# Kernel optimization log

Measured on AMD Instinct MI355X. Metric: run time of the kernel, lower is better.

Reference implementation:

```python
import jax, jax.numpy as jnp
import numpy as np

# __init__ hyperparameters (defaults)
TRACE_BINS = 24
SMOOTH_KERNEL = 5
PAUSE_ENERGY_STD = -0.5
PAUSE_DELTA_Q = 0.35
VOICED_STD = -0.1
BOUNDARY_Q = 0.75

B, T, MEL = 64, 8000, 80


def _sliding_mean(x, k):
    """avg_pool1d(stride=1, padding=k//2, count_include_pad=True) via cumsum. x: [B,T]."""
    pad = k // 2
    xp = jnp.pad(x, ((0, 0), (pad, pad)))
    c = jnp.pad(jnp.cumsum(xp, axis=1), ((0, 0), (1, 0)))
    return (c[:, k:] - c[:, :-k]) / k


def _run_mean(mask):
    """Mean length of runs of True in mask [B,T] = (#ones)/(#runs), 0 if no runs."""
    prev_off = jnp.pad(~mask[:, :-1], ((0, 0), (1, 0)), constant_values=True)
    starts = mask & prev_off
    n_runs = starts.sum(axis=1).astype(jnp.float32)
    ones = mask.sum(axis=1).astype(jnp.float32)
    return jnp.where(n_runs > 0, ones / jnp.maximum(n_runs, 1.0), 0.0)


def setup_inputs() -> dict:
    key = jax.random.key(0)
    ref_mel = jax.random.normal(key, (B, T, MEL), dtype=jnp.float32)
    return {"ref_mel": ref_mel}


def reference(ref_mel):
    b, t, _ = ref_mel.shape
    energy = ref_mel.mean(axis=-1)                                  # [B,T]
    mu = energy.mean(axis=1, keepdims=True)
    sd = jnp.maximum(energy.std(axis=1, keepdims=True, ddof=1), 1e-6)  # torch.std is unbiased
    z = (energy - mu) / sd

    delta = jnp.pad(jnp.abs(energy[:, 1:] - energy[:, :-1]), ((0, 0), (1, 0)))
    dthr = jnp.quantile(delta, PAUSE_DELTA_Q, axis=1, keepdims=True)
    pause = (z <= PAUSE_ENERGY_STD) & (delta <= dthr)
    speech = ~pause
    voiced = (z > VOICED_STD).astype(jnp.float32)

    k = min(SMOOTH_KERNEL, max(1, t))
    local_rate = _sliding_mean(delta, k)[:, :t]
    k2 = min(k + 2, max(1, t))
    boundary_strength = _sliding_mean(delta, k2)[:, :t]

    sp = jnp.cumsum(speech.astype(jnp.float32), axis=1)
    total = jnp.maximum(sp[:, -1:], 1.0)
    progress = sp / total                                           # [B,T], nondecreasing
    uniform = jnp.linspace(0.0, 1.0, t)[None, :]
    seg_bias = progress - uniform

    bthr = jnp.quantile(boundary_strength, BOUNDARY_Q, axis=1, keepdims=True)
    bev = (boundary_strength >= bthr).astype(jnp.float32)

    feat = jnp.stack([pause.astype(jnp.float32), local_rate, bev, seg_bias, voiced], axis=-1)  # [B,T,5]

    # progress-based resampling: parallel binary search + gather + lerp
    target = jnp.linspace(0.0, 1.0, TRACE_BINS)
    right = jax.vmap(lambda p: jnp.searchsorted(p, target, side='left'))(progress)  # [B,bins]
    left = jnp.clip(right - 1, 0, t - 1)
    rc = jnp.clip(right, 0, t - 1)
    pl = jnp.take_along_axis(progress, left, axis=1)
    pr = jnp.take_along_axis(progress, rc, axis=1)
    denom = jnp.maximum(jnp.abs(pr - pl), 1e-6)
    alpha = jnp.clip((target[None, :] - pl) / denom, 0.0, 1.0)
    alpha = jnp.where(right <= 0, 0.0, jnp.where(right >= t, 1.0, alpha))[..., None]  # [B,bins,1]
    fdim = feat.shape[-1]
    li = jnp.broadcast_to(left[:, :, None], (b, TRACE_BINS, fdim))
    ri = jnp.broadcast_to(rc[:, :, None], (b, TRACE_BINS, fdim))
    fl = jnp.take_along_axis(feat, li, axis=1)
    fr = jnp.take_along_axis(feat, ri, axis=1)
    trace = fl * (1.0 - alpha) + fr * alpha                          # [B,bins,5]

    stats = jnp.stack([
        pause.astype(jnp.float32).mean(axis=1),
        _run_mean(pause),
        _run_mean(speech),
        local_rate[:, -1] - local_rate[:, 0],
        bev.mean(axis=1),
        voiced.mean(axis=1),
    ], axis=-1)                                                      # [B,6]
    return stats, trace
```

## Files before the change

kernel.cpp:

```cpp
#include <hip/hip_runtime.h>
#include <hip/hip_bf16.h>

#define TT 8000
#define BB 64
#define NBINS 24
#define CAP 256
#define NS 8
#define NHB 1024

__global__ __launch_bounds__(256) void k_energy(const float* __restrict__ mel,
                                                double* __restrict__ e_bt){
  __shared__ float sm[5120];
  const int blk = blockIdx.x, tid = threadIdx.x;
  const float4* g = (const float4*)(mel + (size_t)blk * 5120);
  float4* s4 = (float4*)sm;
  #pragma unroll
  for (int j = 0; j < 5; ++j) s4[tid + j * 256] = g[tid + j * 256];
  __syncthreads();
  const float* p = sm + tid * 20;
  double s = 0.0;
  #pragma unroll
  for (int j = 0; j < 20; ++j) s += (double)p[j];
  s += __shfl_xor(s, 1, 64);
  s += __shfl_xor(s, 2, 64);
  if ((tid & 3) == 0) e_bt[(size_t)blk * 64 + (tid >> 2)] = s / 80.0;
}

#define QUANT(VALS, RNK, OUTIDX, QG, MAXIDX)                                     \
  {                                                                              \
    const double maxv = scD[MAXIDX];                                             \
    if (maxv <= 0.0){                                                            \
      if (tid == 0) scD[OUTIDX] = 0.0;                                           \
      __syncthreads();                                                           \
    } else {                                                                     \
      const double scale = (double)NHB / maxv;                                   \
      if (tid < 8) scI[tid] = 0;                                                 \
      hist[tid] = 0;                                                             \
      __syncthreads();                                                           \
      _Pragma("unroll")                                                          \
      for (int s = 0; s < NS; ++s){                                              \
        int t = tid + (s << 10);                                                 \
        if (t < TT){                                                             \
          int bi = (int)(VALS[s] * scale); if (bi > NHB-1) bi = NHB-1;           \
          atomicAdd(&hist[bi], 1);                                               \
        }                                                                        \
      }                                                                          \
      __syncthreads();                                                           \
      const int h = hist[tid];                                                   \
      int inc = h;                                                               \
      _Pragma("unroll")                                                          \
      for (int d2 = 1; d2 < 64; d2 <<= 1){                                       \
        int nb = __shfl_up(inc, d2, 64);                                         \
        if (lane >= d2) inc += nb;                                               \
      }                                                                          \
      if (lane == 63) waveTot[wid] = inc;                                        \
      __syncthreads();                                                           \
      if (tid == 0){                                                             \
        int acc = 0;                                                             \
        for (int w2 = 0; w2 < 16; ++w2){ waveOff[w2] = acc; acc += waveTot[w2]; } \
      }                                                                          \
      __syncthreads();                                                           \
      {                                                                          \
        int P = waveOff[wid] + inc;            \
        if ((RNK)   >= P - h && (RNK)   < P){ scI[0] = tid; scI[2] = P - h; }    \
        if ((RNK)+1 >= P - h && (RNK)+1 < P){ scI[1] = tid; scI[3] = P; }        \
      }                                                                          \
      __syncthreads();                                                           \
      const int binr = scI[0], binr1 = scI[1], Pm = scI[2];                      \
      const int cwin = scI[3] - scI[2];                                          \
      if (cwin <= CAP){                                                          \
        _Pragma("unroll")                                                        \
        for (int s = 0; s < NS; ++s){                                            \
          int t = tid + (s << 10);                                               \
          if (t < TT){                                                           \
            int bi = (int)(VALS[s] * scale); if (bi > NHB-1) bi = NHB-1;         \
            if (bi >= binr && bi <= binr1){                                      \
              int ix = atomicAdd(&scI[4], 1);                                    \
              if (ix < CAP) cand[ix] = VALS[s];                                  \
            }                                                                    \
          }                                                                      \
        }                                                                        \
        __syncthreads();                                                         \
        int n = scI[4]; if (n > CAP) n = CAP;                                    \
        int tgt = (RNK) - Pm;                                                    \
        if (tid < n){                                                            \
          double mv = cand[tid];                                                 \
          int rk = 0;                                                            \
          for (int j = 0; j < n; ++j){ double cj = cand[j];                      \
            rk += (cj < mv || (cj == mv && j < tid)) ? 1 : 0; }                  \
          if (rk == tgt)     scD[4] = mv;                                        \
          if (rk == tgt + 1) scD[5] = mv;                                        \
        }                                                                        \
        __syncthreads();                                                         \
      } else {                                                                   \
                           \
        double lo_ = -0.5, hi_ = maxv;                                           \
        int cl_ = 0, ch_ = 8000;                                                 \
        for (;;){                                                                \
          if (ch_ - cl_ <= CAP){                                                 \
            if (tid == 0) scI[5] = 0;                                            \
            __syncthreads();                                                     \
            _Pragma("unroll")                                                    \
            for (int s = 0; s < NS; ++s){                                        \
              int t = tid + (s << 10);                                           \
              if (t < TT){ double v = VALS[s];                                   \
                if (v > lo_ && v <= hi_){ int ix = atomicAdd(&scI[5], 1);        \
                  if (ix < CAP) cand[ix] = v; } }                                \
            }                                                                    \
            __syncthreads();                                                     \
            int n = scI[5]; if (n > CAP) n = CAP;                                \
            int tgt = (RNK) - cl_;                                               \
            if (tid < n){                                                        \
              double mv = cand[tid];                                             \
              int rk = 0;                                                        \
              for (int j = 0; j < n; ++j){ double cj = cand[j];                  \
                rk += (cj < mv || (cj == mv && j < tid)) ? 1 : 0; }              \
              if (rk == tgt)     scD[4] = mv;                                    \
              if (rk == tgt + 1) scD[5] = mv;                                    \
            }                                                                    \
            __syncthreads();                                                     \
            break;                                                               \
          }                                                                      \
          double mid_ = 0.5 * (lo_ + hi_);                                       \
          if (!(mid_ > lo_ && mid_ < hi_)){                                      \
            if (tid == 0){ scD[4] = hi_; scD[5] = hi_; }                         \
            __syncthreads();                                                     \
            break;                                                               \
          }                                                                      \
          int c_ = 0;                                                            \
          _Pragma("unroll")                                                      \
          for (int s = 0; s < NS; ++s){                                          \
            int t = tid + (s << 10);                                             \
            if (t < TT && VALS[s] <= mid_) c_++;                                 \
          }                                                                      \
          _Pragma("unroll")                                                      \
          for (int o = 32; o; o >>= 1) c_ += __shfl_down(c_, o, 64);             \
          if (lane == 0) redI[wid] = c_;                                         \
          __syncthreads();                                                       \
          if (tid == 0){ int a = 0; for (int i = 0; i < 16; ++i) a += redI[i]; scI[6] = a; } \
          __syncthreads();                                                       \
          int ct_ = scI[6];                                                      \
          if (ct_ <= (RNK)){ lo_ = mid_; cl_ = ct_; }                            \
          else if (ct_ >= (RNK) + 2){ hi_ = mid_; ch_ = ct_; }                   \
          else {                                                                 \
            double mx_ = -1.0, mn_ = 1e300;                                      \
            _Pragma("unroll")                                                    \
            for (int s = 0; s < NS; ++s){                                        \
              int t = tid + (s << 10);                                           \
              if (t < TT){ double v = VALS[s];                                   \
                if (v <= mid_){ if (v > mx_) mx_ = v; } else { if (v < mn_) mn_ = v; } } \
            }                                                                    \
            _Pragma("unroll")                                                    \
            for (int o = 32; o; o >>= 1){ double x = __shfl_down(mx_, o, 64); if (x > mx_) mx_ = x; } \
            if (lane == 0) redD[wid] = mx_;                                      \
            __syncthreads();                                                     \
            if (tid == 0){ double a = redD[0]; for (int i = 1; i < 16; ++i) if (redD[i] > a) a = redD[i]; scD[4] = a; } \
            __syncthreads();                                                     \
            _Pragma("unroll")                                                    \
            for (int o = 32; o; o >>= 1){ double x = __shfl_down(mn_, o, 64); if (x < mn_) mn_ = x; } \
            if (lane == 0) redD[wid] = mn_;                                      \
            __syncthreads();                                                     \
            if (tid == 0){ double a = redD[0]; for (int i = 1; i < 16; ++i) if (redD[i] < a) a = redD[i]; scD[5] = a; } \
            __syncthreads();                                                     \
            break;                                                               \
          }                                                                      \
        }                                                                        \
      }                                                                          \
      if (tid == 0){                                                             \
        double d_ = scD[5] - scD[4];                                             \
        double g_ = (QG);                                                        \
        scD[OUTIDX] = (g_ >= 0.5) ? (scD[5] - d_ * (1.0 - g_)) : (scD[4] + d_ * g_); \
      }                                                                          \
      __syncthreads();                                                           \
    }                                                                            \
  }

__global__ __launch_bounds__(1024) void k_row(const double* __restrict__ e_all,
                                              float* __restrict__ out){
  __shared__ double e_s[TT];
  __shared__ double delta_s[TT];
  __shared__ __align__(16) unsigned short runs[TT];
  __shared__ unsigned char flags[TT];
  __shared__ double cand[CAP];
  __shared__ double redD[64];
  __shared__ int    redI[16];
  __shared__ double scD[12];
  __shared__ int    scI[8];
  __shared__ int    waveTot[16], waveOff[16], cnt5[5];
  int* hist = (int*)runs;

  const int b = blockIdx.x, tid = threadIdx.x;
  const int lane = tid & 63, wid = tid >> 6;
  const double* eg = e_all + (size_t)b * TT;

  if (tid < 5) cnt5[tid] = 0;

  double ev[NS], dv[NS], bv[NS];
  #pragma unroll
  for (int s = 0; s < NS; ++s){
    int t = tid + (s << 10);
    double e = (t < TT) ? eg[t] : 0.0;
    ev[s] = e;
    if (t < TT) e_s[t] = e;
  }
  __syncthreads();
  #pragma unroll
  for (int s = 0; s < NS; ++s){
    int t = tid + (s << 10);
    double d = 0.0;
    if (t > 0 && t < TT) d = fabs(e_s[t] - e_s[t-1]);
    dv[s] = d;
    if (t < TT) delta_s[t] = d;
  }
  __syncthreads();
  #pragma unroll
  for (int s = 0; s < NS; ++s){
    int t = tid + (s << 10);
    double sum = 0.0;
    if (t < TT){
      int j0 = t - 3; if (j0 < 0) j0 = 0;
      int j1 = t + 3; if (j1 > TT-1) j1 = TT-1;
      for (int j = j0; j <= j1; ++j) sum += delta_s[j];
    }
    bv[s] = sum / 7.0;
  }
  {
    double se = 0.0, s2 = 0.0, md = 0.0, mb = 0.0;
    #pragma unroll
    for (int s = 0; s < NS; ++s){
      se += ev[s]; s2 += ev[s] * ev[s];
      if (dv[s] > md) md = dv[s];
      if (bv[s] > mb) mb = bv[s];
    }
    #pragma unroll
    for (int o = 32; o; o >>= 1){
      se += __shfl_down(se, o, 64);
      s2 += __shfl_down(s2, o, 64);
      double x = __shfl_down(md, o, 64); if (x > md) md = x;
      x = __shfl_down(mb, o, 64); if (x > mb) mb = x;
    }
    if (lane == 0){ redD[wid] = se; redD[16+wid] = s2; redD[32+wid] = md; redD[48+wid] = mb; }
    __syncthreads();
    if (tid == 0){
      double a = 0, q = 0, c = 0, d2 = 0;
      for (int i = 0; i < 16; ++i){
        a += redD[i]; q += redD[16+i];
        if (redD[32+i] > c) c = redD[32+i];
        if (redD[48+i] > d2) d2 = redD[48+i];
      }
      double mu0 = a / 8000.0;
      double var = (q - a * a / 8000.0) / 7999.0;
      if (var < 0.0) var = 0.0;
      double sd0 = sqrt(var); if (sd0 < 1e-6) sd0 = 1e-6;
      scD[0] = mu0; scD[1] = sd0; scD[6] = c; scD[7] = d2;
    }
    __syncthreads();
  }
  const double mu = scD[0], sd = scD[1];

  QUANT(dv, 2799, 2, (0.35 * 7999.0 - 2799.0), 6);
  QUANT(bv, 5999, 3, (0.75 * 7999.0 - 5999.0), 7);
  const double dthr = scD[2], bthr = scD[3];

  #pragma unroll
  for (int s = 0; s < NS; ++s){
    int t = tid + (s << 10);
    if (t < TT){
      double z = (ev[s] - mu) / sd;
      bool pause  = (z <= -0.5) && (dv[s] <= dthr);
      bool voiced = (z > -0.1);
      bool bev    = (bv[s] >= bthr);
      flags[t] = (unsigned char)((pause ? 1 : 0) | (voiced ? 2 : 0) | (bev ? 4 : 0));
    }
  }
  __syncthreads();
  {
    int cp = 0, crp = 0, crs = 0, cv = 0, cb = 0;
    #pragma unroll
    for (int s = 0; s < NS; ++s){
      int t = tid + (s << 10);
      if (t < TT){
        unsigned f = flags[t];
        bool pause = (f & 1) != 0;
        bool prevP = (t > 0) ? ((flags[t-1] & 1) != 0) : false;
        cp += pause ? 1 : 0; cv += (f >> 1) & 1; cb += (f >> 2) & 1;
        if (pause && (t == 0 || !prevP)) crp++;
        if (!pause && (t == 0 || prevP)) crs++;
      }
    }
    #pragma unroll
    for (int o = 32; o; o >>= 1){
      cp += __shfl_down(cp, o, 64); crp += __shfl_down(crp, o, 64);
      crs += __shfl_down(crs, o, 64); cv += __shfl_down(cv, o, 64);
      cb += __shfl_down(cb, o, 64);
    }
    if (lane == 0){
      atomicAdd(&cnt5[0], cp); atomicAdd(&cnt5[1], crp); atomicAdd(&cnt5[2], crs);
      atomicAdd(&cnt5[3], cv); atomicAdd(&cnt5[4], cb);
    }
  }
  const int t0 = tid * 8;
  int local_speech = 0;
  if (t0 < TT){
    #pragma unroll
    for (int k = 0; k < 8; ++k) local_speech += (flags[t0 + k] & 1) ? 0 : 1;
  }
  int inc = local_speech;
  #pragma unroll
  for (int d = 1; d < 64; d <<= 1){
    int nb = __shfl_up(inc, d, 64);
    if (lane >= d) inc += nb;
  }
  if (lane == 63) waveTot[wid] = inc;
  __syncthreads();
  if (tid == 0){
    int acc = 0;
    for (int w2 = 0; w2 < 16; ++w2){ waveOff[w2] = acc; acc += waveTot[w2]; }
    scD[8] = (acc > 1) ? (double)acc : 1.0;
  }
  __syncthreads();
  const double tf = scD[8];
  if (t0 < TT){
    int run = waveOff[wid] + (inc - local_speech);
    #pragma unroll
    for (int k = 0; k < 8; ++k){
      int t = t0 + k;
      run += (flags[t] & 1) ? 0 : 1;
      runs[t] = (unsigned short)run;
    }
  }
  __syncthreads();
  if (tid == 0){
    float onesP = (float)cnt5[0];
    float onesS = (float)(TT - cnt5[0]);
    float* st = out + b * 6;
    st[0] = onesP / 8000.0f;
    st[1] = (cnt5[1] > 0) ? (onesP / fmaxf((float)cnt5[1], 1.0f)) : 0.0f;
    st[2] = (cnt5[2] > 0) ? (onesS / fmaxf((float)cnt5[2], 1.0f)) : 0.0f;
    st[3] = (float)((delta_s[7997] + delta_s[7998] + delta_s[7999]) / 5.0
                  - (delta_s[0] + delta_s[1] + delta_s[2]) / 5.0);
    st[4] = ((float)cnt5[4]) / 8000.0f;
    st[5] = ((float)cnt5[3]) / 8000.0f;
  }
  if (tid < NBINS){
    double target = (tid == NBINS - 1) ? 1.0 : (double)tid * (1.0 / 23.0);
    int lo2 = 0, hi2 = TT;
    while (lo2 < hi2){
      int mid = (lo2 + hi2) >> 1;
      if ((double)runs[mid] / tf < target) lo2 = mid + 1; else hi2 = mid;
    }
    int right = lo2;
    int li = right - 1; if (li < 0) li = 0; if (li > TT-1) li = TT-1;
    int ri = right;     if (ri < 0) ri = 0; if (ri > TT-1) ri = TT-1;
    double pl = (double)runs[li] / tf, pr = (double)runs[ri] / tf;
    double denom = fabs(pr - pl); if (denom < 1e-6) denom = 1e-6;
    double alpha = (target - pl) / denom;
    if (alpha < 0.0) alpha = 0.0;
    if (alpha > 1.0) alpha = 1.0;
    if (right <= 0) alpha = 0.0;
    else if (right >= TT) alpha = 1.0;
    double fL[5], fR[5];
    for (int sdx = 0; sdx < 2; ++sdx){
      int i = sdx ? ri : li;
      double* f = sdx ? fR : fL;
      unsigned fl = flags[i];
      int j0 = i - 2; if (j0 < 0) j0 = 0;
      int j1 = i + 2; if (j1 > TT-1) j1 = TT-1;
      double ws = 0.0;
      for (int j = j0; j <= j1; ++j) ws += delta_s[j];
      f[0] = (fl & 1) ? 1.0 : 0.0;
      f[1] = ws / 5.0;
      f[2] = (fl & 4) ? 1.0 : 0.0;
      double u = (i == TT - 1) ? 1.0 : (double)i * (1.0 / 7999.0);
      f[3] = (double)runs[i] / tf - u;
      f[4] = (fl & 2) ? 1.0 : 0.0;
    }
    double om = 1.0 - alpha;
    float* tr = out + BB * 6 + ((size_t)b * NBINS + tid) * 5;
    #pragma unroll
    for (int f = 0; f < 5; ++f)
      tr[f] = (float)(fL[f] * om + fR[f] * alpha);
  }
}

extern "C" void kernel_launch(void* const* d_in, const int* in_sizes, int n_in,
                              void* d_out, int out_size, void* d_ws, size_t ws_size,
                              hipStream_t stream){
  const float* mel = (const float*)d_in[0];
  float* out = (float*)d_out;
  double* e_bt = (double*)d_ws;

  hipLaunchKernelGGL(k_energy, dim3(8000), dim3(256),  0, stream, mel, e_bt);
  hipLaunchKernelGGL(k_row,    dim3(BB),   dim3(1024), 0, stream, e_bt, out);
}
```

Measured before the change: 53.39 us.

## Merge both quantile histogram passes and shrink row kernel to 512 threads

The per-row kernel now runs 512 threads with 16 elements each. The two quantile selections (delta and boundary strength) share one histogram build, prefix scan, candidate gather and rank pass instead of running back-to-back, which roughly halves the number of block barriers. Cross-wave reductions now use a shuffle within one wave instead of a serial loop on thread 0. The histogram is smaller (512 bins), so more candidates can land in a bin and push selection onto the slower bisection fallback. Fewer threads per row also means less parallelism on the 64 row blocks.

```diff
diff --git a/kernel.cpp b/kernel.cpp
--- a/kernel.cpp
+++ b/kernel.cpp
@@ -5,8 +5,9 @@
 #define BB 64
 #define NBINS 24
 #define CAP 256
-#define NS 8
-#define NHB 1024
+#define NT 512
+#define NS 16
+#define NHB 512
 
 __global__ __launch_bounds__(256) void k_energy(const float* __restrict__ mel,
                                                 double* __restrict__ e_bt){
@@ -26,179 +27,109 @@
   if ((tid & 3) == 0) e_bt[(size_t)blk * 64 + (tid >> 2)] = s / 80.0;
 }
 
-#define QUANT(VALS, RNK, OUTIDX, QG, MAXIDX)                                     \
+#define FALLBACK(VALS, RNK, OUTLO, MAXV, CBASE)                                  \
   {                                                                              \
-    const double maxv = scD[MAXIDX];                                             \
-    if (maxv <= 0.0){                                                            \
-      if (tid == 0) scD[OUTIDX] = 0.0;                                           \
-      __syncthreads();                                                           \
-    } else {                                                                     \
-      const double scale = (double)NHB / maxv;                                   \
-      if (tid < 8) scI[tid] = 0;                                                 \
-      hist[tid] = 0;                                                             \
-      __syncthreads();                                                           \
+    double lo_ = -0.5, hi_ = (MAXV);                                             \
+    int cl_ = 0, ch_ = 8000;                                                     \
+    for (;;){                                                                    \
+      if (ch_ - cl_ <= CAP){                                                     \
+        if (tid == 0) redI[0] = 0;                                               \
+        __syncthreads();                                                         \
+        _Pragma("unroll")                                                        \
+        for (int s = 0; s < NS; ++s){                                            \
+          int t = tid + (s << 9);                                                \
+          if (t < TT){ double v = VALS[s];                                       \
+            if (v > lo_ && v <= hi_){ int ix = atomicAdd(&redI[0], 1);           \
+              if (ix < CAP) cand[(CBASE) + ix] = v; } }                          \
+        }                                                                        \
+        __syncthreads();                                                         \
+        int n = redI[0]; if (n > CAP) n = CAP;                                   \
+        int tgt = (RNK) - cl_;                                                   \
+        if (tid < n){                                                            \
+          double mv = cand[(CBASE) + tid];                                       \
+          int rk = 0;                                                            \
+          for (int j = 0; j < n; ++j){ double cj = cand[(CBASE) + j];            \
+            rk += (cj < mv || (cj == mv && j < tid)) ? 1 : 0; }                  \
+          if (rk == tgt)     scD[OUTLO] = mv;                                    \
+          if (rk == tgt + 1) scD[(OUTLO) + 1] = mv;                              \
+        }                                                                        \
+        __syncthreads();                                                         \
+        break;                                                                   \
+      }                                                                          \
+      double mid_ = 0.5 * (lo_ + hi_);                                           \
+      if (!(mid_ > lo_ && mid_ < hi_)){                                          \
+        if (tid == 0){ scD[OUTLO] = hi_; scD[(OUTLO) + 1] = hi_; }               \
+        __syncthreads();                                                         \
+        break;                                                                   \
+      }                                                                          \
+      int c_ = 0;                                                                \
       _Pragma("unroll")                                                          \
       for (int s = 0; s < NS; ++s){                                              \
-        int t = tid + (s << 10);                                                 \
-        if (t < TT){                                                             \
-          int bi = (int)(VALS[s] * scale); if (bi > NHB-1) bi = NHB-1;           \
-          atomicAdd(&hist[bi], 1);                                               \
-        }                                                                        \
+        int t = tid + (s << 9);                                                  \
+        if (t < TT && VALS[s] <= mid_) c_++;                                     \
       }                                                                          \
+      _Pragma("unroll")                                                          \
+      for (int o = 32; o; o >>= 1) c_ += __shfl_down(c_, o, 64);                 \
+      if (lane == 0) redI[wid] = c_;                                             \
       __syncthreads();                                                           \
-      const int h = hist[tid];                                                   \
-      int inc = h;                                                               \
-      _Pragma("unroll")                                                          \
-      for (int d2 = 1; d2 < 64; d2 <<= 1){                                       \
-        int nb = __shfl_up(inc, d2, 64);                                         \
-        if (lane >= d2) inc += nb;                                               \
-      }                                                                          \
-      if (lane == 63) waveTot[wid] = inc;                                        \
+      if (tid == 0){ int a2 = 0; for (int i = 0; i < 8; ++i) a2 += redI[i]; scI[5] = a2; } \
       __syncthreads();                                                           \
-      if (tid == 0){                                                             \
-        int acc = 0;                                                             \
-        for (int w2 = 0; w2 < 16; ++w2){ waveOff[w2] = acc; acc += waveTot[w2]; } \
-      }                                                                          \
-      __syncthreads();                                                           \
-      {                                                                          \
-        int P = waveOff[wid] + inc;            \
-        if ((RNK)   >= P - h && (RNK)   < P){ scI[0] = tid; scI[2] = P - h; }    \
-        if ((RNK)+1 >= P - h && (RNK)+1 < P){ scI[1] = tid; scI[3] = P; }        \
-      }                                                                          \
-      __syncthreads();                                                           \
-      const int binr = scI[0], binr1 = scI[1], Pm = scI[2];                      \
-      const int cwin = scI[3] - scI[2];                                          \
-      if (cwin <= CAP){                                                          \
+      int ct_ = scI[5];                                                          \
+      if (ct_ <= (RNK)){ lo_ = mid_; cl_ = ct_; }                                \
+      else if (ct_ >= (RNK) + 2){ hi_ = mid_; ch_ = ct_; }                       \
+      else {                                                                     \
+        double mx_ = -1.0, mn_ = 1e300;                                          \
         _Pragma("unroll")                                                        \
         for (int s = 0; s < NS; ++s){                                            \
-          int t = tid + (s << 10);                                               \
-          if (t < TT){                                                           \
-            int bi = (int)(VALS[s] * scale); if (bi > NHB-1) bi = NHB-1;         \
-            if (bi >= binr && bi <= binr1){                                      \
-              int ix = atomicAdd(&scI[4], 1);                                    \
-              if (ix < CAP) cand[ix] = VALS[s];                                  \
-            }                                                                    \
-          }                                                                      \
+          int t = tid + (s << 9);                                                \
+          if (t < TT){ double v = VALS[s];                                       \
+            if (v <= mid_){ if (v > mx_) mx_ = v; } else { if (v < mn_) mn_ = v; } } \
         }                                                                        \
-        __syncthreads();                                                         \
-        int n = scI[4]; if (n > CAP) n = CAP;                                    \
-        int tgt = (RNK) - Pm;                                                    \
-        if (tid < n){                                                            \
-          double mv = cand[tid];                                                 \
-          int rk = 0;                                                            \
-          for (int j = 0; j < n; ++j){ double cj = cand[j];                      \
-            rk += (cj < mv || (cj == mv && j < tid)) ? 1 : 0; }                  \
-          if (rk == tgt)     scD[4] = mv;                                        \
-          if (rk == tgt + 1) scD[5] = mv;                                        \
-        }                                                                        \
-        __syncthreads();                                                         \
-      } else {                                                                   \
-                           \
-        double lo_ = -0.5, hi_ = maxv;                                           \
-        int cl_ = 0, ch_ = 8000;                                                 \
-        for (;;){                                                                \
-          if (ch_ - cl_ <= CAP){                                                 \
-            if (tid == 0) scI[5] = 0;                                            \
-            __syncthreads();                                                     \
-            _Pragma("unroll")                                                    \
-            for (int s = 0; s < NS; ++s){                                        \
-              int t = tid + (s << 10);                                           \
-              if (t < TT){ double v = VALS[s];                                   \
-                if (v > lo_ && v <= hi_){ int ix = atomicAdd(&scI[5], 1);        \
-                  if (ix < CAP) cand[ix] = v; } }                                \
-            }                                                                    \
-            __syncthreads();                                                     \
-            int n = scI[5]; if (n > CAP) n = CAP;                                \
-            int tgt = (RNK) - cl_;                                               \
-            if (tid < n){                                                        \
-              double mv = cand[tid];                                             \
-              int rk = 0;                                                        \
-              for (int j = 0; j < n; ++j){ double cj = cand[j];                  \
-                rk += (cj < mv || (cj == mv && j < tid)) ? 1 : 0; }              \
-              if (rk == tgt)     scD[4] = mv;                                    \
-              if (rk == tgt + 1) scD[5] = mv;                                    \
-            }                                                                    \
-            __syncthreads();                                                     \
-            break;                                                               \
-          }                                                                      \
-          double mid_ = 0.5 * (lo_ + hi_);                                       \
-          if (!(mid_ > lo_ && mid_ < hi_)){                                      \
-            if (tid == 0){ scD[4] = hi_; scD[5] = hi_; }                         \
-            __syncthreads();                                                     \
-            break;                                                               \
-          }                                                                      \
-          int c_ = 0;                                                            \
-          _Pragma("unroll")                                                      \
-          for (int s = 0; s < NS; ++s){                                          \
-            int t = tid + (s << 10);                                             \
-            if (t < TT && VALS[s] <= mid_) c_++;                                 \
-          }                                                                      \
-          _Pragma("unroll")                                                      \
-          for (int o = 32; o; o >>= 1) c_ += __shfl_down(c_, o, 64);             \
-          if (lane == 0) redI[wid] = c_;                                         \
-          __syncthreads();                                                       \
-          if (tid == 0){ int a = 0; for (int i = 0; i < 16; ++i) a += redI[i]; scI[6] = a; } \
-          __syncthreads();                                                       \
-          int ct_ = scI[6];                                                      \
-          if (ct_ <= (RNK)){ lo_ = mid_; cl_ = ct_; }                            \
-          else if (ct_ >= (RNK) + 2){ hi_ = mid_; ch_ = ct_; }                   \
-          else {                                                                 \
-            double mx_ = -1.0, mn_ = 1e300;                                      \
-            _Pragma("unroll")                                                    \
-            for (int s = 0; s < NS; ++s){                                        \
-              int t = tid + (s << 10);                                           \
-              if (t < TT){ double v = VALS[s];                                   \
-                if (v <= mid_){ if (v > mx_) mx_ = v; } else { if (v < mn_) mn_ = v; } } \
-            }                                                                    \
-            _Pragma("unroll")                                                    \
-            for (int o = 32; o; o >>= 1){ double x = __shfl_down(mx_, o, 64); if (x > mx_) mx_ = x; } \
-            if (lane == 0) redD[wid] = mx_;                                      \
-            __syncthreads();                                                     \
-            if (tid == 0){ double a = redD[0]; for (int i = 1; i < 16; ++i) if (redD[i] > a) a = redD[i]; scD[4] = a; } \
-            __syncthreads();                                                     \
-            _Pragma("unroll")                                                    \
-            for (int o = 32; o; o >>= 1){ double x = __shfl_down(mn_, o, 64); if (x < mn_) mn_ = x; } \
-            if (lane == 0) redD[wid] = mn_;                                      \
-            __syncthreads();                                                     \
-            if (tid == 0){ double a = redD[0]; for (int i = 1; i < 16; ++i) if (redD[i] < a) a = redD[i]; scD[5] = a; } \
-            __syncthreads();                                                     \
-            break;                                                               \
-          }                                                                      \
-        }                                                                        \
+        _Pragma("unroll")                                                        \
+        for (int o = 32; o; o >>= 1){ double x = __shfl_down(mx_, o, 64); if (x > mx_) mx_ = x; } \
+        if (lane == 0) redD[wid] = mx_;                                          \
+        __syncthreads();                                                         \
+        if (tid == 0){ double a2 = redD[0]; for (int i = 1; i < 8; ++i) if (redD[i] > a2) a2 = redD[i]; scD[OUTLO] = a2; } \
+        __syncthreads();                                                         \
+        _Pragma("unroll")                                                        \
+        for (int o = 32; o; o >>= 1){ double x = __shfl_down(mn_, o, 64); if (x < mn_) mn_ = x; } \
+        if (lane == 0) redD[wid] = mn_;                                          \
+        __syncthreads();                                                         \
+        if (tid == 0){ double a2 = redD[0]; for (int i = 1; i < 8; ++i) if (redD[i] < a2) a2 = redD[i]; scD[(OUTLO) + 1] = a2; } \
+        __syncthreads();                                                         \
+        break;                                                                   \
       }                                                                          \
-      if (tid == 0){                                                             \
-        double d_ = scD[5] - scD[4];                                             \
-        double g_ = (QG);                                                        \
-        scD[OUTIDX] = (g_ >= 0.5) ? (scD[5] - d_ * (1.0 - g_)) : (scD[4] + d_ * g_); \
-      }                                                                          \
-      __syncthreads();                                                           \
     }                                                                            \
   }
 
-__global__ __launch_bounds__(1024) void k_row(const double* __restrict__ e_all,
-                                              float* __restrict__ out){
+__global__ __launch_bounds__(NT) void k_row(const double* __restrict__ e_all,
+                                            float* __restrict__ out){
   __shared__ double e_s[TT];
   __shared__ double delta_s[TT];
   __shared__ __align__(16) unsigned short runs[TT];
   __shared__ unsigned char flags[TT];
-  __shared__ double cand[CAP];
-  __shared__ double redD[64];
-  __shared__ int    redI[16];
+  __shared__ double cand[2 * CAP];
+  __shared__ double redD[32];
+  __shared__ int    redI[8];
   __shared__ double scD[12];
-  __shared__ int    scI[8];
-  __shared__ int    waveTot[16], waveOff[16], cnt5[5];
-  int* hist = (int*)runs;
+  __shared__ int    scI[16];
+  __shared__ int    wTD[8], wOD[8], wTB[8], wOB[8], wT[8], wO[8];
+  __shared__ int    cnt5[5];
+  int* histD = (int*)runs;
+  int* histB = histD + NHB;
 
   const int b = blockIdx.x, tid = threadIdx.x;
   const int lane = tid & 63, wid = tid >> 6;
   const double* eg = e_all + (size_t)b * TT;
 
   if (tid < 5) cnt5[tid] = 0;
+  if (tid < 16) scI[tid] = 0;
+  histD[tid] = 0; histB[tid] = 0;
 
   double ev[NS], dv[NS], bv[NS];
   #pragma unroll
   for (int s = 0; s < NS; ++s){
-    int t = tid + (s << 10);
+    int t = tid + (s << 9);
     double e = (t < TT) ? eg[t] : 0.0;
     ev[s] = e;
     if (t < TT) e_s[t] = e;
@@ -206,7 +137,7 @@
   __syncthreads();
   #pragma unroll
   for (int s = 0; s < NS; ++s){
-    int t = tid + (s << 10);
+    int t = tid + (s << 9);
     double d = 0.0;
     if (t > 0 && t < TT) d = fabs(e_s[t] - e_s[t-1]);
     dv[s] = d;
@@ -215,7 +146,7 @@
   __syncthreads();
   #pragma unroll
   for (int s = 0; s < NS; ++s){
-    int t = tid + (s << 10);
+    int t = tid + (s << 9);
     double sum = 0.0;
     if (t < TT){
       int j0 = t - 3; if (j0 < 0) j0 = 0;
@@ -239,32 +170,135 @@
       double x = __shfl_down(md, o, 64); if (x > md) md = x;
       x = __shfl_down(mb, o, 64); if (x > mb) mb = x;
     }
-    if (lane == 0){ redD[wid] = se; redD[16+wid] = s2; redD[32+wid] = md; redD[48+wid] = mb; }
-    __syncthreads();
-    if (tid == 0){
-      double a = 0, q = 0, c = 0, d2 = 0;
-      for (int i = 0; i < 16; ++i){
-        a += redD[i]; q += redD[16+i];
-        if (redD[32+i] > c) c = redD[32+i];
-        if (redD[48+i] > d2) d2 = redD[48+i];
-      }
+    if (lane == 0){ redD[wid] = se; redD[8+wid] = s2; redD[16+wid] = md; redD[24+wid] = mb; }
+  }
+  __syncthreads();
+  if (tid < 64){
+    double a = (lane < 8) ? redD[lane]      : 0.0;
+    double q = (lane < 8) ? redD[8 + lane]  : 0.0;
+    double c = (lane < 8) ? redD[16 + lane] : 0.0;
+    double d = (lane < 8) ? redD[24 + lane] : 0.0;
+    #pragma unroll
+    for (int o = 4; o; o >>= 1){
+      a += __shfl_down(a, o, 64);
+      q += __shfl_down(q, o, 64);
+      double x = __shfl_down(c, o, 64); if (x > c) c = x;
+      x = __shfl_down(d, o, 64); if (x > d) d = x;
+    }
+    if (lane == 0){
       double mu0 = a / 8000.0;
       double var = (q - a * a / 8000.0) / 7999.0;
       if (var < 0.0) var = 0.0;
       double sd0 = sqrt(var); if (sd0 < 1e-6) sd0 = 1e-6;
-      scD[0] = mu0; scD[1] = sd0; scD[6] = c; scD[7] = d2;
-    }
-    __syncthreads();
-  }
+      scD[0] = mu0; scD[1] = sd0; scD[9] = c; scD[10] = d;
+    }
+  }
+  __syncthreads();
   const double mu = scD[0], sd = scD[1];
-
-  QUANT(dv, 2799, 2, (0.35 * 7999.0 - 2799.0), 6);
-  QUANT(bv, 5999, 3, (0.75 * 7999.0 - 5999.0), 7);
+  const double maxd = scD[9], maxb = scD[10];
+  const bool doD = (maxd > 0.0), doB = (maxb > 0.0);
+  const double sclD = doD ? (double)NHB / maxd : 0.0;
+  const double sclB = doB ? (double)NHB / maxb : 0.0;
+  #pragma unroll
+  for (int s = 0; s < NS; ++s){
+    int t = tid + (s << 9);
+    if (t < TT){
+      if (doD){ int bi = (int)(dv[s] * sclD); if (bi > NHB-1) bi = NHB-1; atomicAdd(&histD[bi], 1); }
+      if (doB){ int bi = (int)(bv[s] * sclB); if (bi > NHB-1) bi = NHB-1; atomicAdd(&histB[bi], 1); }
+    }
+  }
+  __syncthreads();
+  const int hD = histD[tid], hB = histB[tid];
+  int incD = hD, incB = hB;
+  #pragma unroll
+  for (int o = 1; o < 64; o <<= 1){
+    int x = __shfl_up(incD, o, 64); if (lane >= o) incD += x;
+    x = __shfl_up(incB, o, 64); if (lane >= o) incB += x;
+  }
+  if (lane == 63){ wTD[wid] = incD; wTB[wid] = incB; }
+  __syncthreads();
+  if (tid < 64){
+    int vD = (lane < 8) ? wTD[lane] : 0;
+    int vB = (lane < 8) ? wTB[lane] : 0;
+    int iD = vD, iB = vB;
+    #pragma unroll
+    for (int o = 1; o < 8; o <<= 1){
+      int x = __shfl_up(iD, o, 64); if (lane >= o) iD += x;
+      x = __shfl_up(iB, o, 64); if (lane >= o) iB += x;
+    }
+    if (lane < 8){ wOD[lane] = iD - vD; wOB[lane] = iB - vB; }
+  }
+  __syncthreads();
+  {
+    int PD = wOD[wid] + incD;
+    int PB = wOB[wid] + incB;
+    if (doD){
+      if (2799 >= PD - hD && 2799 < PD){ scI[0] = tid; scI[2] = PD - hD; }
+      if (2800 >= PD - hD && 2800 < PD){ scI[1] = tid; scI[3] = PD; }
+    }
+    if (doB){
+      if (5999 >= PB - hB && 5999 < PB){ scI[8]  = tid; scI[10] = PB - hB; }
+      if (6000 >= PB - hB && 6000 < PB){ scI[9]  = tid; scI[11] = PB; }
+    }
+  }
+  __syncthreads();
+  const int binrD = scI[0], binr1D = scI[1], PmD = scI[2], cwinD = scI[3] - scI[2];
+  const int binrB = scI[8], binr1B = scI[9], PmB = scI[10], cwinB = scI[11] - scI[10];
+  const bool fastD = doD && (cwinD <= CAP);
+  const bool fastB = doB && (cwinB <= CAP);
+  #pragma unroll
+  for (int s = 0; s < NS; ++s){
+    int t = tid + (s << 9);
+    if (t < TT){
+      if (fastD){
+        int bi = (int)(dv[s] * sclD); if (bi > NHB-1) bi = NHB-1;
+        if (bi >= binrD && bi <= binr1D){ int ix = atomicAdd(&scI[4], 1); if (ix < CAP) cand[ix] = dv[s]; }
+      }
+      if (fastB){
+        int bi = (int)(bv[s] * sclB); if (bi > NHB-1) bi = NHB-1;
+        if (bi >= binrB && bi <= binr1B){ int ix = atomicAdd(&scI[12], 1); if (ix < CAP) cand[CAP + ix] = bv[s]; }
+      }
+    }
+  }
+  __syncthreads();
+  if (fastD){
+    int n = scI[4]; if (n > CAP) n = CAP;
+    int tgt = 2799 - PmD;
+    if (tid < n){
+      double mv = cand[tid];
+      int rk = 0;
+      for (int j = 0; j < n; ++j){ double cj = cand[j]; rk += (cj < mv || (cj == mv && j < tid)) ? 1 : 0; }
+      if (rk == tgt)     scD[4] = mv;
+      if (rk == tgt + 1) scD[5] = mv;
+    }
+  }
+  if (fastB){
+    int n = scI[12]; if (n > CAP) n = CAP;
+    int tgt = 5999 - PmB;
+    if (tid < n){
+      double mv = cand[CAP + tid];
+      int rk = 0;
+      for (int j = 0; j < n; ++j){ double cj = cand[CAP + j]; rk += (cj < mv || (cj == mv && j < tid)) ? 1 : 0; }
+      if (rk == tgt)     scD[6] = mv;
+      if (rk == tgt + 1) scD[7] = mv;
+    }
+  }
+  __syncthreads();
+  if (doD && !fastD){ FALLBACK(dv, 2799, 4, maxd, 0) }
+  if (doB && !fastB){ FALLBACK(bv, 5999, 6, maxb, CAP) }
+  if (tid == 0){
+    double gD = 0.35 * 7999.0 - 2799.0;
+    double dd = scD[5] - scD[4];
+    scD[2] = doD ? ((gD >= 0.5) ? (scD[5] - dd * (1.0 - gD)) : (scD[4] + dd * gD)) : 0.0;
+    double gB = 0.75 * 7999.0 - 5999.0;
+    double db = scD[7] - scD[6];
+    scD[3] = doB ? ((gB >= 0.5) ? (scD[7] - db * (1.0 - gB)) : (scD[6] + db * gB)) : 0.0;
+  }
+  __syncthreads();
   const double dthr = scD[2], bthr = scD[3];
-
-  #pragma unroll
-  for (int s = 0; s < NS; ++s){
-    int t = tid + (s << 10);
+  #pragma unroll
+  for (int s = 0; s < NS; ++s){
+    int t = tid + (s << 9);
     if (t < TT){
       double z = (ev[s] - mu) / sd;
       bool pause  = (z <= -0.5) && (dv[s] <= dthr);
@@ -278,7 +312,7 @@
     int cp = 0, crp = 0, crs = 0, cv = 0, cb = 0;
     #pragma unroll
     for (int s = 0; s < NS; ++s){
-      int t = tid + (s << 10);
+      int t = tid + (s << 9);
       if (t < TT){
         unsigned f = flags[t];
         bool pause = (f & 1) != 0;
@@ -299,34 +333,31 @@
       atomicAdd(&cnt5[3], cv); atomicAdd(&cnt5[4], cb);
     }
   }
-  const int t0 = tid * 8;
-  int local_speech = 0;
-  if (t0 < TT){
-    #pragma unroll
-    for (int k = 0; k < 8; ++k) local_speech += (flags[t0 + k] & 1) ? 0 : 1;
-  }
-  int inc = local_speech;
-  #pragma unroll
-  for (int d = 1; d < 64; d <<= 1){
-    int nb = __shfl_up(inc, d, 64);
-    if (lane >= d) inc += nb;
-  }
-  if (lane == 63) waveTot[wid] = inc;
-  __syncthreads();
-  if (tid == 0){
-    int acc = 0;
-    for (int w2 = 0; w2 < 16; ++w2){ waveOff[w2] = acc; acc += waveTot[w2]; }
-    scD[8] = (acc > 1) ? (double)acc : 1.0;
+  const int t0 = tid * 16;
+  int ls = 0;
+  #pragma unroll
+  for (int k = 0; k < 16; ++k){ int t = t0 + k; if (t < TT) ls += (flags[t] & 1) ? 0 : 1; }
+  int inc = ls;
+  #pragma unroll
+  for (int o = 1; o < 64; o <<= 1){ int x = __shfl_up(inc, o, 64); if (lane >= o) inc += x; }
+  if (lane == 63) wT[wid] = inc;
+  __syncthreads();
+  if (tid < 64){
+    int v = (lane < 8) ? wT[lane] : 0;
+    int i2 = v;
+    #pragma unroll
+    for (int o = 1; o < 8; o <<= 1){ int x = __shfl_up(i2, o, 64); if (lane >= o) i2 += x; }
+    if (lane < 8) wO[lane] = i2 - v;
+    if (lane == 7) scD[8] = (i2 > 1) ? (double)i2 : 1.0;
   }
   __syncthreads();
   const double tf = scD[8];
-  if (t0 < TT){
-    int run = waveOff[wid] + (inc - local_speech);
-    #pragma unroll
-    for (int k = 0; k < 8; ++k){
+  {
+    int run = wO[wid] + (inc - ls);
+    #pragma unroll
+    for (int k = 0; k < 16; ++k){
       int t = t0 + k;
-      run += (flags[t] & 1) ? 0 : 1;
-      runs[t] = (unsigned short)run;
+      if (t < TT){ run += (flags[t] & 1) ? 0 : 1; runs[t] = (unsigned short)run; }
     }
   }
   __syncthreads();
@@ -390,6 +421,6 @@
   float* out = (float*)d_out;
   double* e_bt = (double*)d_ws;
 
-  hipLaunchKernelGGL(k_energy, dim3(8000), dim3(256),  0, stream, mel, e_bt);
-  hipLaunchKernelGGL(k_row,    dim3(BB),   dim3(1024), 0, stream, e_bt, out);
+  hipLaunchKernelGGL(k_energy, dim3(8000), dim3(256), 0, stream, mel, e_bt);
+  hipLaunchKernelGGL(k_row,    dim3(BB),   dim3(NT),  0, stream, e_bt, out);
 }
```

Measured after the change: 57.28 us. 1.07x slower.
